# Optimization experiments

Measured on AMD Instinct MI355X. Metric: run time of the kernel, lower is better.

## Reference

```python
import jax, jax.numpy as jnp
import numpy as np

N, F_IN, HEADS, F_OUT = 4096, 128, 4, 32
DENSITY = 0.05


def setup_inputs() -> dict:
    key = jax.random.key(0)
    k_x, k_adj, k_w, k_as, k_ad, k_b = jax.random.split(key, 6)
    x = jax.random.normal(k_x, (N, F_IN), dtype=jnp.float32)
    # binary adjacency with self-loops so every row of Tau_sum is nonzero
    adj = (jax.random.uniform(k_adj, (N, N)) < DENSITY).astype(jnp.float32)
    adj = jnp.maximum(adj, jnp.eye(N, dtype=jnp.float32))
    weight = jax.random.normal(k_w, (HEADS * F_OUT, F_IN), dtype=jnp.float32) * 0.1
    att_src = jax.random.normal(k_as, (1, HEADS, F_OUT), dtype=jnp.float32) * 0.1
    att_dst = jax.random.normal(k_ad, (1, HEADS, F_OUT), dtype=jnp.float32) * 0.1
    bias = jax.random.normal(k_b, (HEADS * F_OUT,), dtype=jnp.float32) * 0.1
    return {"x": x, "adj_matrix": adj, "weight": weight,
            "att_src": att_src, "att_dst": att_dst, "bias": bias}


def reference(x, adj_matrix, weight, att_src, att_dst, bias):
    n = x.shape[0]
    heads = att_src.shape[1]
    f_out = weight.shape[0] // heads
    # H' = x W^T, reshaped to [N, heads, F_out]
    h_prime = (x @ weight.T).reshape(n, heads, f_out)
    alpha_src = jnp.sum(h_prime * att_src, axis=-1)  # [N, heads]
    alpha_dst = jnp.sum(h_prime * att_dst, axis=-1)  # [N, heads]
    # C[m, n, h] = alpha_src[n, h] + alpha_dst[m, h]
    C = alpha_src[None, :, :] + alpha_dst[:, None, :]
    adj_t = adj_matrix.T[..., None]                  # [N, N, 1]
    # exp(leaky_relu(C, 0.2)) masked by adjacency
    tau = adj_t * jnp.exp(jnp.maximum(0.2 * C, C))   # [N, N, heads]
    tau_sum = jnp.sum(tau, axis=1, keepdims=True)    # [N, 1, heads]
    att_weights = tau / tau_sum
    # Z[m, h, f] = sum_n (adjT * att)[m, n, h] * H'[n, h, f]
    z = jnp.einsum('mnh,nhf->mhf', adj_t * att_weights, h_prime)
    return z.reshape(n, heads * f_out) + bias
```

## Files before the change

kernel.cpp:

```cpp
#include <hip/hip_runtime.h>
#include <hip/hip_bf16.h>

#define N_NODES 4096
#define F_IN    128
#define HEADS   4
#define FTOT    128
#define CAP     512
#define LCAP    48
#define HPB     512
#define SCB     1024

__global__ __launch_bounds__(256)
void k_pre(const float* __restrict__ x, const float* __restrict__ W,
           const float* __restrict__ att_src, const float* __restrict__ att_dst,
           const float* __restrict__ adj,
           __hip_bfloat16* __restrict__ hpb, float* __restrict__ as_,
           float* __restrict__ ad_, int* __restrict__ cnt,
           unsigned short* __restrict__ lists)
{
    const int t = threadIdx.x;
    if (blockIdx.x < HPB) {
        __shared__ float xs[8 * F_IN];
        const int sub = t >> 7;
        const int tt  = t & 127;
        const int i0  = blockIdx.x * 8 + sub * 4;
        reinterpret_cast<float4*>(xs)[t] =
            reinterpret_cast<const float4*>(x + (size_t)blockIdx.x * 8 * F_IN)[t];
        __syncthreads();

        const float4* W4  = reinterpret_cast<const float4*>(W + tt * F_IN);
        const float4* xs4 = reinterpret_cast<const float4*>(xs + sub * 4 * F_IN);
        float a0 = 0.f, a1 = 0.f, a2 = 0.f, a3 = 0.f;
#pragma unroll
        for (int k = 0; k < F_IN / 4; ++k) {
            const float4 w  = W4[k];
            const float4 v0 = xs4[k], v1 = xs4[32 + k], v2 = xs4[64 + k], v3 = xs4[96 + k];
            a0 = fmaf(w.x, v0.x, a0); a0 = fmaf(w.y, v0.y, a0); a0 = fmaf(w.z, v0.z, a0); a0 = fmaf(w.w, v0.w, a0);
            a1 = fmaf(w.x, v1.x, a1); a1 = fmaf(w.y, v1.y, a1); a1 = fmaf(w.z, v1.z, a1); a1 = fmaf(w.w, v1.w, a1);
            a2 = fmaf(w.x, v2.x, a2); a2 = fmaf(w.y, v2.y, a2); a2 = fmaf(w.z, v2.z, a2); a2 = fmaf(w.w, v2.w, a2);
            a3 = fmaf(w.x, v3.x, a3); a3 = fmaf(w.y, v3.y, a3); a3 = fmaf(w.z, v3.z, a3); a3 = fmaf(w.w, v3.w, a3);
        }
        hpb[(size_t)(i0 + 0) * FTOT + tt] = __float2bfloat16(a0);
        hpb[(size_t)(i0 + 1) * FTOT + tt] = __float2bfloat16(a1);
        hpb[(size_t)(i0 + 2) * FTOT + tt] = __float2bfloat16(a2);
        hpb[(size_t)(i0 + 3) * FTOT + tt] = __float2bfloat16(a3);

        const float asv = att_src[tt], adv = att_dst[tt];
        float s0 = a0 * asv, s1 = a1 * asv, s2 = a2 * asv, s3 = a3 * asv;
        float d0 = a0 * adv, d1 = a1 * adv, d2 = a2 * adv, d3 = a3 * adv;
#pragma unroll
        for (int s = 16; s; s >>= 1) {
            s0 += __shfl_xor(s0, s); s1 += __shfl_xor(s1, s);
            s2 += __shfl_xor(s2, s); s3 += __shfl_xor(s3, s);
            d0 += __shfl_xor(d0, s); d1 += __shfl_xor(d1, s);
            d2 += __shfl_xor(d2, s); d3 += __shfl_xor(d3, s);
        }
        if ((tt & 31) == 0) {
            const int hh = tt >> 5;
            as_[(i0 + 0) * HEADS + hh] = s0; as_[(i0 + 1) * HEADS + hh] = s1;
            as_[(i0 + 2) * HEADS + hh] = s2; as_[(i0 + 3) * HEADS + hh] = s3;
            ad_[(i0 + 0) * HEADS + hh] = d0; ad_[(i0 + 1) * HEADS + hh] = d1;
            ad_[(i0 + 2) * HEADS + hh] = d2; ad_[(i0 + 3) * HEADS + hh] = d3;
        }
    } else {
        __shared__ int lcnt[64];
        __shared__ int gbase[64];
        __shared__ unsigned short lbuf[64][LCAP];
        const int sblk  = blockIdx.x - HPB;
        const int strip = sblk & 63;
        const int chunk = sblk >> 6;
        const int c0    = strip * 64;
        const int r0    = chunk * 256;
        const int q     = t & 15;
        const int p     = t >> 4;
        if (t < 64) lcnt[t] = 0;
        __syncthreads();

        const float4* adj4 = reinterpret_cast<const float4*>(adj);
        float4 v[16];
#pragma unroll
        for (int it = 0; it < 16; ++it)
            v[it] = adj4[(size_t)(r0 + p + it * 16) * (N_NODES / 4) + (c0 >> 2) + q];

        unsigned mk0 = 0, mk1 = 0, mk2 = 0, mk3 = 0;
#pragma unroll
        for (int it = 0; it < 16; ++it) {
            mk0 |= (v[it].x != 0.f) ? (1u << it) : 0u;
            mk1 |= (v[it].y != 0.f) ? (1u << it) : 0u;
            mk2 |= (v[it].z != 0.f) ? (1u << it) : 0u;
            mk3 |= (v[it].w != 0.f) ? (1u << it) : 0u;
        }
        unsigned mks[4] = {mk0, mk1, mk2, mk3};
#pragma unroll
        for (int j = 0; j < 4; ++j) {
            unsigned mask = mks[j];
            if (mask) {
                const int ml = 4 * q + j;
                int slot = atomicAdd(&lcnt[ml], __popc(mask));
                while (mask) {
                    const int it = __ffs(mask) - 1;
                    mask &= mask - 1;
                    lbuf[ml][slot++] = (unsigned short)(r0 + p + it * 16);
                }
            }
        }
        __syncthreads();
        if (t < 64) gbase[t] = atomicAdd(&cnt[c0 + t], lcnt[t]);
        __syncthreads();
        const int ml  = t >> 2;
        const int sub = t & 3;
        const int nn  = lcnt[ml];
        unsigned short* dst = lists + (size_t)(c0 + ml) * CAP + gbase[ml];
        for (int j = sub; j < nn; j += 4) dst[j] = lbuf[ml][j];
    }
}

__global__ __launch_bounds__(256)
void k_agg(const unsigned* __restrict__ hpw, const float* __restrict__ as_,
           const float* __restrict__ ad_, const int* __restrict__ cnt,
           const unsigned short* __restrict__ lists,
           const float* __restrict__ bias, float* __restrict__ out)
{
    __shared__ float e_s[4][64][4];
    __shared__ float mrg[2][32][5];
    const int t    = threadIdx.x;
    const int wv   = t >> 6;
    const int ms   = wv >> 1;
    const int wp   = wv & 1;
    const int l    = t & 63;
    const int m    = blockIdx.x * 2 + ms;
    const int half = l >> 5;
    const int l32  = l & 31;
    const int h    = l32 >> 3;

    const int2 c2    = reinterpret_cast<const int2*>(cnt)[blockIdx.x];
    const int  cm    = ms ? c2.y : c2.x;
    const int  chalf = (cm + 1) >> 1;
    const int  begin = wp ? chalf : 0;
    const int  end   = wp ? cm : chalf;

    const float4 adm = reinterpret_cast<const float4*>(ad_)[m];
    const unsigned short* lst = lists + (size_t)m * CAP;
    const uint2* hp2 = reinterpret_cast<const uint2*>(hpw);
    const float4* as4 = reinterpret_cast<const float4*>(as_);

    float4 acc = make_float4(0.f, 0.f, 0.f, 0.f);
    float tau = 0.f;

    const int nbat = (end - begin + 63) >> 6;
    for (int b = 0; b < nbat; ++b) {
        const int k0 = begin + b * 64;
        const bool valid = (k0 + l) < end;
        const int myidx = valid ? (int)lst[k0 + l] : 0;
        const float4 a = as4[myidx];
        float4 e4;
        const float cx = a.x + adm.x, cy = a.y + adm.y, cz = a.z + adm.z, cw = a.w + adm.w;
        e4.x = valid ? __expf(fmaxf(0.2f * cx, cx)) : 0.f;
        e4.y = valid ? __expf(fmaxf(0.2f * cy, cy)) : 0.f;
        e4.z = valid ? __expf(fmaxf(0.2f * cz, cz)) : 0.f;
        e4.w = valid ? __expf(fmaxf(0.2f * cw, cw)) : 0.f;
        *reinterpret_cast<float4*>(&e_s[wv][l][0]) = e4;
        __builtin_amdgcn_wave_barrier();

        const int rem   = min(64, end - k0);
        const int pairs = (rem + 1) >> 1;
#pragma unroll 8
        for (int j = 0; j < pairs; ++j) {
            const int src = 2 * j + half;
            const int n   = __shfl(myidx, src);
            const float e = e_s[wv][src][h];
            const uint2 u = hp2[(size_t)n * (FTOT / 4) + l32];
            const float f0 = __uint_as_float(u.x << 16);
            const float f1 = __uint_as_float(u.x & 0xffff0000u);
            const float f2 = __uint_as_float(u.y << 16);
            const float f3 = __uint_as_float(u.y & 0xffff0000u);
            acc.x = fmaf(e, f0, acc.x);
            acc.y = fmaf(e, f1, acc.y);
            acc.z = fmaf(e, f2, acc.z);
            acc.w = fmaf(e, f3, acc.w);
            tau += e;
        }
    }

    acc.x += __shfl_xor(acc.x, 32);
    acc.y += __shfl_xor(acc.y, 32);
    acc.z += __shfl_xor(acc.z, 32);
    acc.w += __shfl_xor(acc.w, 32);
    tau   += __shfl_xor(tau, 32);

    if (wp == 1 && half == 0) {
        mrg[ms][l32][0] = acc.x; mrg[ms][l32][1] = acc.y;
        mrg[ms][l32][2] = acc.z; mrg[ms][l32][3] = acc.w;
        mrg[ms][l32][4] = tau;
    }
    __syncthreads();
    if (wp == 0 && half == 0) {
        acc.x += mrg[ms][l32][0]; acc.y += mrg[ms][l32][1];
        acc.z += mrg[ms][l32][2]; acc.w += mrg[ms][l32][3];
        tau   += mrg[ms][l32][4];
        const float inv = 1.f / tau;
        const float4 bv = reinterpret_cast<const float4*>(bias)[l32];
        float4 o;
        o.x = acc.x * inv + bv.x; o.y = acc.y * inv + bv.y;
        o.z = acc.z * inv + bv.z; o.w = acc.w * inv + bv.w;
        reinterpret_cast<float4*>(out)[(size_t)m * (FTOT / 4) + l32] = o;
    }
}

extern "C" void kernel_launch(void* const* d_in, const int* in_sizes, int n_in,
                              void* d_out, int out_size, void* d_ws, size_t ws_size,
                              hipStream_t stream) {
    const float* x       = (const float*)d_in[0];
    const float* adj     = (const float*)d_in[1];
    const float* weight  = (const float*)d_in[2];
    const float* att_src = (const float*)d_in[3];
    const float* att_dst = (const float*)d_in[4];
    const float* bias    = (const float*)d_in[5];
    float* out = (float*)d_out;

    __hip_bfloat16* hpb = (__hip_bfloat16*)d_ws;
    float* as_ = (float*)(hpb + (size_t)N_NODES * FTOT);
    float* ad_ = as_ + (size_t)N_NODES * HEADS;
    int*   cnt = (int*)(ad_ + (size_t)N_NODES * HEADS);
    unsigned short* lists = (unsigned short*)(cnt + N_NODES);

    hipMemsetAsync(cnt, 0, N_NODES * sizeof(int), stream);
    k_pre<<<HPB + SCB, 256, 0, stream>>>(x, weight, att_src, att_dst, adj,
                                         hpb, as_, ad_, cnt, lists);
    k_agg<<<N_NODES / 2, 256, 0, stream>>>((const unsigned*)hpb, as_, ad_, cnt,
                                           lists, bias, out);
}
```

Baseline: 51.67 us.

## Store per-chunk neighbor segments with counts instead of atomic global compaction

Each scan block now writes its neighbor list into a fixed per-chunk slot and stores a 16-bit count per (column, chunk), replacing the global atomicAdd offset reservation, the extra __syncthreads, and the memset of the counter array. The aggregation kernel reads the 16 chunk counts, builds prefix sums over the 8 chunks each wave handles, and maps each lane's position to a segment and offset. This removes one memset launch and global atomics. In exchange it adds per-lane segment lookup work and a sparser, larger list layout. The work split between the two waves now depends on chunk counts rather than an exact half.

Result: faster. 49.69 us (-3.8%).

```diff
diff --git a/kernel.cpp b/kernel.cpp
--- a/kernel.cpp
+++ b/kernel.cpp
@@ -5,8 +5,9 @@
 #define F_IN    128
 #define HEADS   4
 #define FTOT    128
-#define CAP     512
+#define NCHUNK  16
 #define LCAP    48
+#define LSTR    (NCHUNK * LCAP)
 #define HPB     512
 #define SCB     1024
 
@@ -15,7 +16,7 @@
            const float* __restrict__ att_src, const float* __restrict__ att_dst,
            const float* __restrict__ adj,
            __hip_bfloat16* __restrict__ hpb, float* __restrict__ as_,
-           float* __restrict__ ad_, int* __restrict__ cnt,
+           float* __restrict__ ad_, unsigned short* __restrict__ cnt16,
            unsigned short* __restrict__ lists)
 {
     const int t = threadIdx.x;
@@ -64,7 +65,6 @@
         }
     } else {
         __shared__ int lcnt[64];
-        __shared__ int gbase[64];
         __shared__ unsigned short lbuf[64][LCAP];
         const int sblk  = blockIdx.x - HPB;
         const int strip = sblk & 63;
@@ -105,19 +105,18 @@
             }
         }
         __syncthreads();
-        if (t < 64) gbase[t] = atomicAdd(&cnt[c0 + t], lcnt[t]);
-        __syncthreads();
+        if (t < 64) cnt16[(size_t)(c0 + t) * NCHUNK + chunk] = (unsigned short)lcnt[t];
         const int ml  = t >> 2;
         const int sub = t & 3;
         const int nn  = lcnt[ml];
-        unsigned short* dst = lists + (size_t)(c0 + ml) * CAP + gbase[ml];
+        unsigned short* dst = lists + (size_t)(c0 + ml) * LSTR + chunk * LCAP;
         for (int j = sub; j < nn; j += 4) dst[j] = lbuf[ml][j];
     }
 }
 
 __global__ __launch_bounds__(256)
 void k_agg(const unsigned* __restrict__ hpw, const float* __restrict__ as_,
-           const float* __restrict__ ad_, const int* __restrict__ cnt,
+           const float* __restrict__ ad_, const unsigned short* __restrict__ cnt16,
            const unsigned short* __restrict__ lists,
            const float* __restrict__ bias, float* __restrict__ out)
 {
@@ -133,36 +132,48 @@
     const int l32  = l & 31;
     const int h    = l32 >> 3;
 
-    const int2 c2    = reinterpret_cast<const int2*>(cnt)[blockIdx.x];
-    const int  cm    = ms ? c2.y : c2.x;
-    const int  chalf = (cm + 1) >> 1;
-    const int  begin = wp ? chalf : 0;
-    const int  end   = wp ? cm : chalf;
+    const int cv = (int)cnt16[(size_t)m * NCHUNK + (l & 15)];
+    int cs[8];
+#pragma unroll
+    for (int j = 0; j < 8; ++j) cs[j] = __shfl(cv, 8 * wp + j);
+    int P[9];
+    P[0] = 0;
+#pragma unroll
+    for (int j = 0; j < 8; ++j) P[j + 1] = P[j] + cs[j];
+    const int cw = P[8];
 
     const float4 adm = reinterpret_cast<const float4*>(ad_)[m];
-    const unsigned short* lst = lists + (size_t)m * CAP;
+    const unsigned short* lst = lists + (size_t)m * LSTR + wp * 8 * LCAP;
     const uint2* hp2 = reinterpret_cast<const uint2*>(hpw);
     const float4* as4 = reinterpret_cast<const float4*>(as_);
 
     float4 acc = make_float4(0.f, 0.f, 0.f, 0.f);
     float tau = 0.f;
 
-    const int nbat = (end - begin + 63) >> 6;
+    const int nbat = (cw + 63) >> 6;
     for (int b = 0; b < nbat; ++b) {
-        const int k0 = begin + b * 64;
-        const bool valid = (k0 + l) < end;
-        const int myidx = valid ? (int)lst[k0 + l] : 0;
+        const int o     = b * 64 + l;
+        const bool valid = o < cw;
+        int seg = 0, base = 0;
+#pragma unroll
+        for (int j = 1; j < 8; ++j) {
+            const bool ge = o >= P[j];
+            seg  = ge ? j    : seg;
+            base = ge ? P[j] : base;
+        }
+        const int rel = o - base;
+        const int myidx = valid ? (int)lst[seg * LCAP + rel] : 0;
         const float4 a = as4[myidx];
         float4 e4;
-        const float cx = a.x + adm.x, cy = a.y + adm.y, cz = a.z + adm.z, cw = a.w + adm.w;
+        const float cx = a.x + adm.x, cy = a.y + adm.y, cz = a.z + adm.z, cw_ = a.w + adm.w;
         e4.x = valid ? __expf(fmaxf(0.2f * cx, cx)) : 0.f;
         e4.y = valid ? __expf(fmaxf(0.2f * cy, cy)) : 0.f;
         e4.z = valid ? __expf(fmaxf(0.2f * cz, cz)) : 0.f;
-        e4.w = valid ? __expf(fmaxf(0.2f * cw, cw)) : 0.f;
+        e4.w = valid ? __expf(fmaxf(0.2f * cw_, cw_)) : 0.f;
         *reinterpret_cast<float4*>(&e_s[wv][l][0]) = e4;
         __builtin_amdgcn_wave_barrier();
 
-        const int rem   = min(64, end - k0);
+        const int rem   = min(64, cw - b * 64);
         const int pairs = (rem + 1) >> 1;
 #pragma unroll 8
         for (int j = 0; j < pairs; ++j) {
@@ -221,12 +232,11 @@
     __hip_bfloat16* hpb = (__hip_bfloat16*)d_ws;
     float* as_ = (float*)(hpb + (size_t)N_NODES * FTOT);
     float* ad_ = as_ + (size_t)N_NODES * HEADS;
-    int*   cnt = (int*)(ad_ + (size_t)N_NODES * HEADS);
-    unsigned short* lists = (unsigned short*)(cnt + N_NODES);
-
-    hipMemsetAsync(cnt, 0, N_NODES * sizeof(int), stream);
+    unsigned short* cnt16 = (unsigned short*)(ad_ + (size_t)N_NODES * HEADS);
+    unsigned short* lists = cnt16 + (size_t)N_NODES * NCHUNK;
+
     k_pre<<<HPB + SCB, 256, 0, stream>>>(x, weight, att_src, att_dst, adj,
-                                         hpb, as_, ad_, cnt, lists);
-    k_agg<<<N_NODES / 2, 256, 0, stream>>>((const unsigned*)hpb, as_, ad_, cnt,
+                                         hpb, as_, ad_, cnt16, lists);
+    k_agg<<<N_NODES / 2, 256, 0, stream>>>((const unsigned*)hpb, as_, ad_, cnt16,
                                            lists, bias, out);
 }
```

## Replace sparse gather aggregation with dense bitmask MFMA attention over split node ranges

Applied to the files above, without the earlier changes.

Drops the per-column neighbor lists and atomics. The adjacency is now packed into a bitmask, and H' is stored transposed in bf16. A dense k_main kernel computes masked exp2 weights for every node pair and accumulates them with 32x32x16 bf16 MFMA. The neighbor dimension is split four ways into partial sums, which a new k_fin kernel reduces, normalizes and adds bias to. This swaps irregular gathers for regular tensor-core work, at the cost of about 20x more arithmetic (dense instead of 5% density), bf16-rounded attention weights, and an extra kernel with partial-sum traffic.

Result: slower. 70.68 us (+36.8%).

```diff
diff --git a/kernel.cpp b/kernel.cpp
--- a/kernel.cpp
+++ b/kernel.cpp
@@ -5,27 +5,39 @@
 #define F_IN    128
 #define HEADS   4
 #define FTOT    128
-#define CAP     512
-#define LCAP    48
+#define NSPLIT  4
+#define NRANGE  (N_NODES / NSPLIT)
+#define NSTEP   (NRANGE / 64)
 #define HPB     512
-#define SCB     1024
+#define BITB    1024
+#define L2E     1.4426950408889634f
+
+typedef __attribute__((ext_vector_type(8)))  short  short8v;
+typedef __attribute__((ext_vector_type(16))) float  float16v;
+
+static __device__ __forceinline__ unsigned f2bfu(float f) {
+    union { __hip_bfloat16 h; unsigned short u; } cv;
+    cv.h = __float2bfloat16(f);
+    return (unsigned)cv.u;
+}
 
 __global__ __launch_bounds__(256)
 void k_pre(const float* __restrict__ x, const float* __restrict__ W,
            const float* __restrict__ att_src, const float* __restrict__ att_dst,
            const float* __restrict__ adj,
-           __hip_bfloat16* __restrict__ hpb, float* __restrict__ as_,
-           float* __restrict__ ad_, int* __restrict__ cnt,
-           unsigned short* __restrict__ lists)
+           unsigned short* __restrict__ hpt, float* __restrict__ ast,
+           float* __restrict__ adt, unsigned* __restrict__ abits)
 {
     const int t = threadIdx.x;
     if (blockIdx.x < HPB) {
-        __shared__ float xs[8 * F_IN];
+        __shared__ alignas(16) float    xs[8 * F_IN];
+        __shared__ alignas(16) unsigned hs[F_IN * 4];
+        __shared__ float ssa[4][8], ssd[4][8];
         const int sub = t >> 7;
         const int tt  = t & 127;
-        const int i0  = blockIdx.x * 8 + sub * 4;
+        const int i0  = blockIdx.x * 8;
         reinterpret_cast<float4*>(xs)[t] =
-            reinterpret_cast<const float4*>(x + (size_t)blockIdx.x * 8 * F_IN)[t];
+            reinterpret_cast<const float4*>(x + (size_t)i0 * F_IN)[t];
         __syncthreads();
 
         const float4* W4  = reinterpret_cast<const float4*>(W + tt * F_IN);
@@ -40,10 +52,8 @@
             a2 = fmaf(w.x, v2.x, a2); a2 = fmaf(w.y, v2.y, a2); a2 = fmaf(w.z, v2.z, a2); a2 = fmaf(w.w, v2.w, a2);
             a3 = fmaf(w.x, v3.x, a3); a3 = fmaf(w.y, v3.y, a3); a3 = fmaf(w.z, v3.z, a3); a3 = fmaf(w.w, v3.w, a3);
         }
-        hpb[(size_t)(i0 + 0) * FTOT + tt] = __float2bfloat16(a0);
-        hpb[(size_t)(i0 + 1) * FTOT + tt] = __float2bfloat16(a1);
-        hpb[(size_t)(i0 + 2) * FTOT + tt] = __float2bfloat16(a2);
-        hpb[(size_t)(i0 + 3) * FTOT + tt] = __float2bfloat16(a3);
+        hs[tt * 4 + sub * 2 + 0] = f2bfu(a0) | (f2bfu(a1) << 16);
+        hs[tt * 4 + sub * 2 + 1] = f2bfu(a2) | (f2bfu(a3) << 16);
 
         const float asv = att_src[tt], adv = att_dst[tt];
         float s0 = a0 * asv, s1 = a1 * asv, s2 = a2 * asv, s3 = a3 * asv;
@@ -57,15 +67,22 @@
         }
         if ((tt & 31) == 0) {
             const int hh = tt >> 5;
-            as_[(i0 + 0) * HEADS + hh] = s0; as_[(i0 + 1) * HEADS + hh] = s1;
-            as_[(i0 + 2) * HEADS + hh] = s2; as_[(i0 + 3) * HEADS + hh] = s3;
-            ad_[(i0 + 0) * HEADS + hh] = d0; ad_[(i0 + 1) * HEADS + hh] = d1;
-            ad_[(i0 + 2) * HEADS + hh] = d2; ad_[(i0 + 3) * HEADS + hh] = d3;
+            ssa[hh][sub * 4 + 0] = s0 * L2E; ssa[hh][sub * 4 + 1] = s1 * L2E;
+            ssa[hh][sub * 4 + 2] = s2 * L2E; ssa[hh][sub * 4 + 3] = s3 * L2E;
+            ssd[hh][sub * 4 + 0] = d0 * L2E; ssd[hh][sub * 4 + 1] = d1 * L2E;
+            ssd[hh][sub * 4 + 2] = d2 * L2E; ssd[hh][sub * 4 + 3] = d3 * L2E;
+        }
+        __syncthreads();
+        if (t < 128)
+            *reinterpret_cast<uint4*>(hpt + (size_t)t * N_NODES + i0) =
+                *reinterpret_cast<const uint4*>(&hs[t * 4]);
+        if (t < 64) {
+            const int sd = t >> 5, hh = (t >> 3) & 3, nn = t & 7;
+            const float v = sd ? ssd[hh][nn] : ssa[hh][nn];
+            (sd ? adt : ast)[hh * N_NODES + i0 + nn] = v;
         }
     } else {
-        __shared__ int lcnt[64];
-        __shared__ int gbase[64];
-        __shared__ unsigned short lbuf[64][LCAP];
+        __shared__ alignas(16) unsigned short lb[64 * 16];
         const int sblk  = blockIdx.x - HPB;
         const int strip = sblk & 63;
         const int chunk = sblk >> 6;
@@ -73,15 +90,12 @@
         const int r0    = chunk * 256;
         const int q     = t & 15;
         const int p     = t >> 4;
-        if (t < 64) lcnt[t] = 0;
-        __syncthreads();
-
         const float4* adj4 = reinterpret_cast<const float4*>(adj);
+
         float4 v[16];
 #pragma unroll
         for (int it = 0; it < 16; ++it)
-            v[it] = adj4[(size_t)(r0 + p + it * 16) * (N_NODES / 4) + (c0 >> 2) + q];
-
+            v[it] = adj4[(size_t)(r0 + p * 16 + it) * (N_NODES / 4) + (c0 >> 2) + q];
         unsigned mk0 = 0, mk1 = 0, mk2 = 0, mk3 = 0;
 #pragma unroll
         for (int it = 0; it < 16; ++it) {
@@ -90,121 +104,141 @@
             mk2 |= (v[it].z != 0.f) ? (1u << it) : 0u;
             mk3 |= (v[it].w != 0.f) ? (1u << it) : 0u;
         }
-        unsigned mks[4] = {mk0, mk1, mk2, mk3};
+        lb[(4 * q + 0) * 16 + p] = (unsigned short)mk0;
+        lb[(4 * q + 1) * 16 + p] = (unsigned short)mk1;
+        lb[(4 * q + 2) * 16 + p] = (unsigned short)mk2;
+        lb[(4 * q + 3) * 16 + p] = (unsigned short)mk3;
+        __syncthreads();
+        const unsigned* lb32 = reinterpret_cast<const unsigned*>(lb);
+#pragma unroll
+        for (int j = 0; j < 2; ++j) {
+            const int w = t + j * 256;
+            const int m = w >> 3, col = w & 7;
+            abits[(size_t)(c0 + m) * (N_NODES / 32) + chunk * 8 + col] = lb32[w];
+        }
+    }
+}
+
+__global__ __launch_bounds__(256)
+void k_main(const unsigned short* __restrict__ hpt, const float* __restrict__ ast,
+            const float* __restrict__ adt, const unsigned* __restrict__ abits,
+            float* __restrict__ z_part, float* __restrict__ taup)
+{
+    __shared__ alignas(16) unsigned short hps[128 * 64];
+    __shared__ alignas(16) unsigned       bts[32 * 32];
+    char* hps_c = reinterpret_cast<char*>(hps);
+    char* bts_c = reinterpret_cast<char*>(bts);
+
+    const int t     = threadIdx.x;
+    const int wv    = t >> 6;
+    const int l     = t & 63;
+    const int np    = l >> 5;
+    const int lm    = l & 31;
+    const int mt    = blockIdx.x >> 2;
+    const int split = blockIdx.x & 3;
+    const int m0    = mt * 32;
+    const int nb0   = split * NRANGE;
+
+    {
+        const int m = t >> 3, part = t & 7;
+        uint4 v = *reinterpret_cast<const uint4*>(
+            abits + (size_t)(m0 + m) * (N_NODES / 32) + split * 32 + part * 4);
+        const unsigned byte = (unsigned)(t * 16) ^ ((m & 7) << 4);
+        *reinterpret_cast<uint4*>(bts_c + byte) = v;
+    }
+    auto stage_hp = [&](int step) {
+        const int nb = nb0 + step * 64;
 #pragma unroll
         for (int j = 0; j < 4; ++j) {
-            unsigned mask = mks[j];
-            if (mask) {
-                const int ml = 4 * q + j;
-                int slot = atomicAdd(&lcnt[ml], __popc(mask));
-                while (mask) {
-                    const int it = __ffs(mask) - 1;
-                    mask &= mask - 1;
-                    lbuf[ml][slot++] = (unsigned short)(r0 + p + it * 16);
-                }
-            }
-        }
-        __syncthreads();
-        if (t < 64) gbase[t] = atomicAdd(&cnt[c0 + t], lcnt[t]);
-        __syncthreads();
-        const int ml  = t >> 2;
-        const int sub = t & 3;
-        const int nn  = lcnt[ml];
-        unsigned short* dst = lists + (size_t)(c0 + ml) * CAP + gbase[ml];
-        for (int j = sub; j < nn; j += 4) dst[j] = lbuf[ml][j];
+            const int lin = t + j * 256;
+            const int f = lin >> 3, part = lin & 7;
+            uint4 v = *reinterpret_cast<const uint4*>(
+                hpt + (size_t)f * N_NODES + nb + part * 8);
+            const unsigned byte = (unsigned)(lin * 16) ^ ((f & 7) << 4);
+            *reinterpret_cast<uint4*>(hps_c + byte) = v;
+        }
+    };
+
+    const float adm = adt[wv * N_NODES + m0 + lm];
+    const float* asw = ast + wv * N_NODES + nb0;
+
+    float16v acc;
+#pragma unroll
+    for (int r = 0; r < 16; ++r) acc[r] = 0.f;
+    float tau = 0.f;
+
+    stage_hp(0);
+    __syncthreads();
+    for (int step = 0;;) {
+        const unsigned baddr = (unsigned)(lm * 128 + step * 8) ^ ((lm & 7) << 4);
+        const unsigned long long b64 =
+            *reinterpret_cast<const unsigned long long*>(bts_c + baddr);
+        const int nb = step * 64;
+#pragma unroll
+        for (int q = 0; q < 4; ++q) {
+            const float* ap = asw + nb + q * 16 + np * 8;
+            const float4 a0 = *reinterpret_cast<const float4*>(ap);
+            const float4 a1 = *reinterpret_cast<const float4*>(ap + 4);
+            const unsigned bb = (unsigned)(b64 >> ((2 * q + np) * 8)) & 0xFFu;
+            auto wq = [&](float a, unsigned bit) {
+                const float c  = a + adm;
+                const float ex = exp2f(fmaxf(0.2f * c, c));
+                const float w  = (bb & bit) ? ex : 0.f;
+                tau += w;
+                return w;
+            };
+            const float w0 = wq(a0.x, 1u),  w1 = wq(a0.y, 2u);
+            const float w2 = wq(a0.z, 4u),  w3 = wq(a0.w, 8u);
+            const float w4 = wq(a1.x, 16u), w5 = wq(a1.y, 32u);
+            const float w6 = wq(a1.z, 64u), w7 = wq(a1.w, 128u);
+            union { short8v v; unsigned u[4]; } af;
+            af.u[0] = f2bfu(w0) | (f2bfu(w1) << 16);
+            af.u[1] = f2bfu(w2) | (f2bfu(w3) << 16);
+            af.u[2] = f2bfu(w4) | (f2bfu(w5) << 16);
+            af.u[3] = f2bfu(w6) | (f2bfu(w7) << 16);
+            const unsigned bofs =
+                (unsigned)((wv * 32 + lm) * 128 + (q * 16 + np * 8) * 2) ^ ((lm & 7) << 4);
+            const short8v bv = *reinterpret_cast<const short8v*>(hps_c + bofs);
+            acc = __builtin_amdgcn_mfma_f32_32x32x16_bf16(af.v, bv, acc, 0, 0, 0);
+        }
+        if (++step == NSTEP) break;
+        __syncthreads();
+        stage_hp(step);
+        __syncthreads();
+    }
+
+    tau += __shfl_xor(tau, 32);
+    if (np == 0)
+        taup[((size_t)split * HEADS + wv) * N_NODES + m0 + lm] = tau;
+    float* zp = z_part + (size_t)split * N_NODES * FTOT;
+#pragma unroll
+    for (int r = 0; r < 16; ++r) {
+        const int row = (r & 3) + 8 * (r >> 2) + 4 * np;
+        zp[(size_t)(m0 + row) * FTOT + wv * 32 + lm] = acc[r];
     }
 }
 
 __global__ __launch_bounds__(256)
-void k_agg(const unsigned* __restrict__ hpw, const float* __restrict__ as_,
-           const float* __restrict__ ad_, const int* __restrict__ cnt,
-           const unsigned short* __restrict__ lists,
+void k_fin(const float* __restrict__ z_part, const float* __restrict__ taup,
            const float* __restrict__ bias, float* __restrict__ out)
 {
-    __shared__ float e_s[4][64][4];
-    __shared__ float mrg[2][32][5];
-    const int t    = threadIdx.x;
-    const int wv   = t >> 6;
-    const int ms   = wv >> 1;
-    const int wp   = wv & 1;
-    const int l    = t & 63;
-    const int m    = blockIdx.x * 2 + ms;
-    const int half = l >> 5;
-    const int l32  = l & 31;
-    const int h    = l32 >> 3;
-
-    const int2 c2    = reinterpret_cast<const int2*>(cnt)[blockIdx.x];
-    const int  cm    = ms ? c2.y : c2.x;
-    const int  chalf = (cm + 1) >> 1;
-    const int  begin = wp ? chalf : 0;
-    const int  end   = wp ? cm : chalf;
-
-    const float4 adm = reinterpret_cast<const float4*>(ad_)[m];
-    const unsigned short* lst = lists + (size_t)m * CAP;
-    const uint2* hp2 = reinterpret_cast<const uint2*>(hpw);
-    const float4* as4 = reinterpret_cast<const float4*>(as_);
-
-    float4 acc = make_float4(0.f, 0.f, 0.f, 0.f);
-    float tau = 0.f;
-
-    const int nbat = (end - begin + 63) >> 6;
-    for (int b = 0; b < nbat; ++b) {
-        const int k0 = begin + b * 64;
-        const bool valid = (k0 + l) < end;
-        const int myidx = valid ? (int)lst[k0 + l] : 0;
-        const float4 a = as4[myidx];
-        float4 e4;
-        const float cx = a.x + adm.x, cy = a.y + adm.y, cz = a.z + adm.z, cw = a.w + adm.w;
-        e4.x = valid ? __expf(fmaxf(0.2f * cx, cx)) : 0.f;
-        e4.y = valid ? __expf(fmaxf(0.2f * cy, cy)) : 0.f;
-        e4.z = valid ? __expf(fmaxf(0.2f * cz, cz)) : 0.f;
-        e4.w = valid ? __expf(fmaxf(0.2f * cw, cw)) : 0.f;
-        *reinterpret_cast<float4*>(&e_s[wv][l][0]) = e4;
-        __builtin_amdgcn_wave_barrier();
-
-        const int rem   = min(64, end - k0);
-        const int pairs = (rem + 1) >> 1;
-#pragma unroll 8
-        for (int j = 0; j < pairs; ++j) {
-            const int src = 2 * j + half;
-            const int n   = __shfl(myidx, src);
-            const float e = e_s[wv][src][h];
-            const uint2 u = hp2[(size_t)n * (FTOT / 4) + l32];
-            const float f0 = __uint_as_float(u.x << 16);
-            const float f1 = __uint_as_float(u.x & 0xffff0000u);
-            const float f2 = __uint_as_float(u.y << 16);
-            const float f3 = __uint_as_float(u.y & 0xffff0000u);
-            acc.x = fmaf(e, f0, acc.x);
-            acc.y = fmaf(e, f1, acc.y);
-            acc.z = fmaf(e, f2, acc.z);
-            acc.w = fmaf(e, f3, acc.w);
-            tau += e;
-        }
-    }
-
-    acc.x += __shfl_xor(acc.x, 32);
-    acc.y += __shfl_xor(acc.y, 32);
-    acc.z += __shfl_xor(acc.z, 32);
-    acc.w += __shfl_xor(acc.w, 32);
-    tau   += __shfl_xor(tau, 32);
-
-    if (wp == 1 && half == 0) {
-        mrg[ms][l32][0] = acc.x; mrg[ms][l32][1] = acc.y;
-        mrg[ms][l32][2] = acc.z; mrg[ms][l32][3] = acc.w;
-        mrg[ms][l32][4] = tau;
-    }
-    __syncthreads();
-    if (wp == 0 && half == 0) {
-        acc.x += mrg[ms][l32][0]; acc.y += mrg[ms][l32][1];
-        acc.z += mrg[ms][l32][2]; acc.w += mrg[ms][l32][3];
-        tau   += mrg[ms][l32][4];
-        const float inv = 1.f / tau;
-        const float4 bv = reinterpret_cast<const float4*>(bias)[l32];
-        float4 o;
-        o.x = acc.x * inv + bv.x; o.y = acc.y * inv + bv.y;
-        o.z = acc.z * inv + bv.z; o.w = acc.w * inv + bv.w;
-        reinterpret_cast<float4*>(out)[(size_t)m * (FTOT / 4) + l32] = o;
-    }
+    const int idx = blockIdx.x * 256 + threadIdx.x;
+    const int m = idx >> 5, f4 = idx & 31, h = f4 >> 3;
+    const float4* zp4 = reinterpret_cast<const float4*>(z_part);
+    float4 z = make_float4(0.f, 0.f, 0.f, 0.f);
+    float ts = 0.f;
+#pragma unroll
+    for (int s = 0; s < NSPLIT; ++s) {
+        const float4 zs = zp4[(size_t)s * N_NODES * (FTOT / 4) + idx];
+        z.x += zs.x; z.y += zs.y; z.z += zs.z; z.w += zs.w;
+        ts += taup[((size_t)s * HEADS + h) * N_NODES + m];
+    }
+    const float inv = 1.f / ts;
+    const float4 b = reinterpret_cast<const float4*>(bias)[f4];
+    float4 o;
+    o.x = z.x * inv + b.x; o.y = z.y * inv + b.y;
+    o.z = z.z * inv + b.z; o.w = z.w * inv + b.w;
+    reinterpret_cast<float4*>(out)[idx] = o;
 }
 
 extern "C" void kernel_launch(void* const* d_in, const int* in_sizes, int n_in,
@@ -218,15 +252,16 @@
     const float* bias    = (const float*)d_in[5];
     float* out = (float*)d_out;
 
-    __hip_bfloat16* hpb = (__hip_bfloat16*)d_ws;
-    float* as_ = (float*)(hpb + (size_t)N_NODES * FTOT);
-    float* ad_ = as_ + (size_t)N_NODES * HEADS;
-    int*   cnt = (int*)(ad_ + (size_t)N_NODES * HEADS);
-    unsigned short* lists = (unsigned short*)(cnt + N_NODES);
-
-    hipMemsetAsync(cnt, 0, N_NODES * sizeof(int), stream);
-    k_pre<<<HPB + SCB, 256, 0, stream>>>(x, weight, att_src, att_dst, adj,
-                                         hpb, as_, ad_, cnt, lists);
-    k_agg<<<N_NODES / 2, 256, 0, stream>>>((const unsigned*)hpb, as_, ad_, cnt,
-                                           lists, bias, out);
-}
+    unsigned short* hpt = (unsigned short*)d_ws;
+    float* ast = (float*)(hpt + (size_t)FTOT * N_NODES);
+    float* adt = ast + (size_t)HEADS * N_NODES;
+    unsigned* abits = (unsigned*)(adt + (size_t)HEADS * N_NODES);
+    float* z_part = (float*)(abits + (size_t)N_NODES * (N_NODES / 32));
+    float* taup = z_part + (size_t)NSPLIT * N_NODES * FTOT;
+
+    k_pre <<<HPB + BITB, 256, 0, stream>>>(x, weight, att_src, att_dst, adj,
+                                           hpt, ast, adt, abits);
+    k_main<<<(N_NODES / 32) * NSPLIT, 256, 0, stream>>>(hpt, ast, adt, abits,
+                                                        z_part, taup);
+    k_fin <<<N_NODES * (FTOT / 4) / 256, 256, 0, stream>>>(z_part, taup, bias, out);
+}
```
